# Optimization experiments

Measured on AMD Instinct MI355X. Metric: run time of the kernel, lower is better.

Reference implementation:

```python
import jax, jax.numpy as jnp
import numpy as np

N_NODES = 50000

def gcn_conv(x, src, dst, W, b, n_nodes):
    # PyG GCNConv: add self-loops, symmetric normalization D^-1/2 (A+I) D^-1/2, then bias
    loop = jnp.arange(n_nodes)
    s = jnp.concatenate([src, loop])
    d = jnp.concatenate([dst, loop])
    deg = jax.ops.segment_sum(jnp.ones(s.shape[0], x.dtype), d, num_segments=n_nodes)
    dinv = jnp.where(deg > 0, jax.lax.rsqrt(deg), 0.0)
    norm = dinv[s] * dinv[d]                      # [E+N]
    h = x @ W                                      # [N, out]
    msg = h[s] * norm[:, None]                     # gather + scale
    out = jax.ops.segment_sum(msg, d, num_segments=n_nodes)  # scatter-add
    return out + b

def setup_inputs() -> dict:
    key = jax.random.key(0)
    ks = jax.random.split(key, 8)
    x = jax.random.normal(ks[0], (N_NODES, 128), jnp.float32)
    edge_index = jax.random.randint(ks[1], (2, 800000), 0, N_NODES)
    def glorot(k, fan_in, fan_out):
        lim = np.sqrt(6.0 / (fan_in + fan_out)).astype(np.float32)
        return jax.random.uniform(k, (fan_in, fan_out), jnp.float32, -lim, lim)
    return {
        "x": x,
        "edge_index": edge_index,
        "conv_w1": glorot(ks[2], 128, 64), "conv_b1": jnp.zeros((64,), jnp.float32),
        "conv_w2": glorot(ks[3], 64, 64),  "conv_b2": jnp.zeros((64,), jnp.float32),
        "fc_w1": glorot(ks[4], 64, 32),    "fc_b1": jnp.zeros((32,), jnp.float32),
        "fc_w2": glorot(ks[5], 32, 1),     "fc_b2": jnp.zeros((1,), jnp.float32),
    }

def reference(x, edge_index, conv_w1, conv_b1, conv_w2, conv_b2, fc_w1, fc_b1, fc_w2, fc_b2):
    src, dst = edge_index[0], edge_index[1]
    h = jnp.tanh(gcn_conv(x, src, dst, conv_w1, conv_b1, N_NODES))
    h = jnp.tanh(gcn_conv(h, src, dst, conv_w2, conv_b2, N_NODES))
    h = jnp.tanh(h @ fc_w1 + fc_b1)  # dropout is identity at inference
    return h @ fc_w2 + fc_b2          # [N, 1]
```

## Files before the change

### kernel.cpp

```cpp
#include <hip/hip_runtime.h>
#include <math.h>

#define TPB 256
#define NBK_MAX 512
#define FILL_CAP 4096
#define SC_CH 16

typedef short bf16x8 __attribute__((ext_vector_type(8)));
typedef float f32x4 __attribute__((ext_vector_type(4)));

__device__ __forceinline__ unsigned short rne_bf16(float f) {
  unsigned u = __float_as_uint(f);
  return (unsigned short)((u + 0x7fffu + ((u >> 16) & 1u)) >> 16);
}
__device__ __forceinline__ float bf16_f(unsigned short v) {
  return __uint_as_float((unsigned)v << 16);
}

__global__ __launch_bounds__(TPB) void k_bcount(const int* __restrict__ dst,
                                                int* __restrict__ btot, int E, int NBK) {
  __shared__ int h[NBK_MAX];
  int tid = threadIdx.x, blk = blockIdx.x, G = gridDim.x;
  for (int b = tid; b < NBK; b += TPB) h[b] = 0;
  __syncthreads();
  int chunk = (E + G - 1) / G, lo = blk * chunk, hi = min(E, lo + chunk);
  for (int e = lo + tid; e < hi; e += TPB) atomicAdd(&h[dst[e] >> 7], 1);
  __syncthreads();
  for (int b = tid; b < NBK; b += TPB)
    if (h[b]) atomicAdd(&btot[b], h[b]);
}

__global__ __launch_bounds__(TPB) void k_bstart(const int* __restrict__ btot,
                                                int* __restrict__ bstart,
                                                int* __restrict__ gcur,
                                                int* __restrict__ rowptr,
                                                int NBK, int N, int E) {
  __shared__ int sc[TPB];
  int t = threadIdx.x;
  int i0 = 2 * t, i1 = 2 * t + 1;
  int a0 = (i0 < NBK) ? btot[i0] : 0;
  int a1 = (i1 < NBK) ? btot[i1] : 0;
  int s = a0 + a1;
  sc[t] = s;
  __syncthreads();
  for (int o = 1; o < TPB; o <<= 1) {
    int v = (t >= o) ? sc[t - o] : 0;
    __syncthreads();
    sc[t] += v;
    __syncthreads();
  }
  int excl = sc[t] - s;
  if (i0 < NBK) { bstart[i0] = excl;      gcur[i0] = excl; }
  if (i1 < NBK) { bstart[i1] = excl + a0; gcur[i1] = excl + a0; }
  if (t == 0) { bstart[NBK] = E; rowptr[N] = E; }
}

__global__ __launch_bounds__(TPB) void k_bscatter(const int* __restrict__ src,
                                                  const int* __restrict__ dst,
                                                  int* __restrict__ gcur,
                                                  unsigned* __restrict__ e2,
                                                  int E, int NBK) {
  __shared__ int h[NBK_MAX];
  __shared__ int base[NBK_MAX];
  int tid = threadIdx.x, blk = blockIdx.x, G = gridDim.x;
  int chunk = (E + G - 1) / G, lo = blk * chunk, hi = min(E, lo + chunk);
  for (int t0 = lo; t0 < hi; t0 += TPB * SC_CH) {
    int sv[SC_CH], dv[SC_CH];
    for (int b = tid; b < NBK; b += TPB) h[b] = 0;
    __syncthreads();
#pragma unroll
    for (int u = 0; u < SC_CH; ++u) {
      int e = t0 + u * TPB + tid;
      if (e < hi) {
        dv[u] = dst[e];
        sv[u] = src[e];
        atomicAdd(&h[dv[u] >> 7], 1);
      } else {
        dv[u] = -1;
      }
    }
    __syncthreads();
    for (int b = tid; b < NBK; b += TPB) {
      int c = h[b];
      base[b] = c ? atomicAdd(&gcur[b], c) : 0;
    }
    __syncthreads();
    for (int b = tid; b < NBK; b += TPB) h[b] = 0;
    __syncthreads();
#pragma unroll
    for (int u = 0; u < SC_CH; ++u) {
      if (dv[u] >= 0) {
        int bk = dv[u] >> 7;
        int r = atomicAdd(&h[bk], 1);
        e2[base[bk] + r] = ((unsigned)sv[u] << 7) | (unsigned)(dv[u] & 127);
      }
    }
    __syncthreads();
  }
}

__global__ __launch_bounds__(TPB) void k_build(const unsigned* __restrict__ e2,
                                               const int* __restrict__ bstart,
                                               int* __restrict__ rowptr,
                                               float* __restrict__ dinv,
                                               int* __restrict__ col, int N) {
  __shared__ int c[128], sc[128], cur[128];
  __shared__ int buf[FILL_CAP];
  int tid = threadIdx.x, b = blockIdx.x;
  int st = bstart[b], en = bstart[b + 1], len = en - st;
  if (tid < 128) c[tid] = 0;
  __syncthreads();
  for (int i = st + tid; i < en; i += TPB) atomicAdd(&c[e2[i] & 127u], 1);
  __syncthreads();
  if (tid < 128) sc[tid] = c[tid];
  __syncthreads();
  for (int o = 1; o < 128; o <<= 1) {
    int v = (tid >= o && tid < 128) ? sc[tid - o] : 0;
    __syncthreads();
    if (tid < 128) sc[tid] += v;
    __syncthreads();
  }
  if (tid < 128) {
    int excl = sc[tid] - c[tid];
    cur[tid] = excl;
    int node = b * 128 + tid;
    if (node < N) {
      rowptr[node] = st + excl;
      dinv[node] = rsqrtf((float)(c[tid] + 1));
    }
  }
  __syncthreads();
  if (len <= FILL_CAP) {
    for (int i = st + tid; i < en; i += TPB) {
      unsigned v = e2[i];
      int p = atomicAdd(&cur[v & 127u], 1);
      buf[p] = (int)(v >> 7);
    }
    __syncthreads();
    for (int i = tid; i < len; i += TPB) col[st + i] = buf[i];
  } else {
    for (int i = st + tid; i < en; i += TPB) {
      unsigned v = e2[i];
      int p = atomicAdd(&cur[v & 127u], 1);
      col[st + p] = (int)(v >> 7);
    }
  }
}

__global__ __launch_bounds__(TPB) void k_wsplit2(const float* __restrict__ W1,
                                                 const float* __restrict__ W2,
                                                 unsigned short* __restrict__ hi1,
                                                 unsigned short* __restrict__ lo1,
                                                 unsigned short* __restrict__ hi2,
                                                 unsigned short* __restrict__ lo2) {
  int i = blockIdx.x * TPB + threadIdx.x;
  if (i < 128 * 64) {
    int k = i >> 6, n = i & 63;
    float w = W1[i];
    unsigned short h = rne_bf16(w);
    hi1[n * 128 + k] = h;
    lo1[n * 128 + k] = rne_bf16(w - bf16_f(h));
  } else if (i < 128 * 64 + 64 * 64) {
    int j = i - 128 * 64;
    int k = j >> 6, n = j & 63;
    float w = W2[j];
    unsigned short h = rne_bf16(w);
    hi2[n * 64 + k] = h;
    lo2[n * 64 + k] = rne_bf16(w - bf16_f(h));
  }
}

template <int K, bool AF32>
__global__ __launch_bounds__(TPB) void k_mm(const void* __restrict__ Ap,
                                            const unsigned short* __restrict__ WThi,
                                            const unsigned short* __restrict__ WTlo,
                                            unsigned short* __restrict__ Hout, int N) {
  constexpr int P = K + 8;
  __shared__ unsigned short sHi[64 * P];
  __shared__ unsigned short sLo[64 * P];
  int tid = threadIdx.x;
  constexpr int CH = 64 * K / 8;
  for (int i = tid; i < CH; i += TPB) {
    int n = i / (K / 8), ko = i % (K / 8);
    *(int4*)(sHi + n * P + ko * 8) = *(const int4*)(WThi + n * K + ko * 8);
    *(int4*)(sLo + n * P + ko * 8) = *(const int4*)(WTlo + n * K + ko * 8);
  }
  __syncthreads();
  int wave = tid >> 6, lane = tid & 63;
  int oct = lane >> 4, l15 = lane & 15;
  int base = blockIdx.x * 64 + wave * 16;
  int arow = base + l15;
  if (arow >= N) arow = N - 1;
  f32x4 acc[4] = {};
#pragma unroll
  for (int s = 0; s < K / 32; ++s) {
    bf16x8 ahi, alo;
    if (AF32) {
      const float* ap = (const float*)Ap + (size_t)arow * K + s * 32 + oct * 8;
      float4 f0 = *(const float4*)ap;
      float4 f1 = *(const float4*)(ap + 4);
      float fv[8] = {f0.x, f0.y, f0.z, f0.w, f1.x, f1.y, f1.z, f1.w};
#pragma unroll
      for (int j = 0; j < 8; ++j) {
        unsigned short hb = rne_bf16(fv[j]);
        ahi[j] = (short)hb;
        alo[j] = (short)rne_bf16(fv[j] - bf16_f(hb));
      }
    } else {
      ahi = *(const bf16x8*)((const unsigned short*)Ap + (size_t)arow * K + s * 32 + oct * 8);
    }
#pragma unroll
    for (int t = 0; t < 4; ++t) {
      bf16x8 bhi = *(const bf16x8*)(sHi + (t * 16 + l15) * P + s * 32 + oct * 8);
      bf16x8 blo = *(const bf16x8*)(sLo + (t * 16 + l15) * P + s * 32 + oct * 8);
      acc[t] = __builtin_amdgcn_mfma_f32_16x16x32_bf16(ahi, bhi, acc[t], 0, 0, 0);
      acc[t] = __builtin_amdgcn_mfma_f32_16x16x32_bf16(ahi, blo, acc[t], 0, 0, 0);
      if (AF32)
        acc[t] = __builtin_amdgcn_mfma_f32_16x16x32_bf16(alo, bhi, acc[t], 0, 0, 0);
    }
  }
#pragma unroll
  for (int r = 0; r < 4; ++r) {
    int row = base + oct * 4 + r;
    if (row < N) {
#pragma unroll
      for (int t = 0; t < 4; ++t)
        Hout[(size_t)row * 64 + t * 16 + l15] = rne_bf16(acc[t][r]);
    }
  }
}

__device__ __forceinline__ float rl_f(float v, int l) {
  return __int_as_float(__builtin_amdgcn_readlane(__float_as_int(v), l));
}

__global__ __launch_bounds__(TPB) void k_agg(const unsigned short* __restrict__ H,
                                             const int* __restrict__ rowptr,
                                             const int* __restrict__ col,
                                             const float* __restrict__ dinv,
                                             const float* __restrict__ bias,
                                             unsigned short* __restrict__ OUT, int N) {
  int i = (blockIdx.x * TPB + threadIdx.x) >> 6;
  int lane = threadIdx.x & 63;
  if (i >= N) return;
  float di = dinv[i];
  float acc = bf16_f(H[((size_t)i << 6) + lane]) * di * di;
  int beg = rowptr[i], end = rowptr[i + 1];
  for (int c0 = beg; c0 < end; c0 += 64) {
    int m = end - c0;
    if (m > 64) m = 64;
    int jj = c0 + lane;
    int sv = col[jj < end ? jj : beg];
    float nv = di * dinv[sv];
    int t = 0;
    for (; t + 8 <= m; t += 8) {
      int s0 = __builtin_amdgcn_readlane(sv, t + 0);
      int s1 = __builtin_amdgcn_readlane(sv, t + 1);
      int s2 = __builtin_amdgcn_readlane(sv, t + 2);
      int s3 = __builtin_amdgcn_readlane(sv, t + 3);
      int s4 = __builtin_amdgcn_readlane(sv, t + 4);
      int s5 = __builtin_amdgcn_readlane(sv, t + 5);
      int s6 = __builtin_amdgcn_readlane(sv, t + 6);
      int s7 = __builtin_amdgcn_readlane(sv, t + 7);
      float h0 = bf16_f(H[((size_t)s0 << 6) + lane]);
      float h1 = bf16_f(H[((size_t)s1 << 6) + lane]);
      float h2 = bf16_f(H[((size_t)s2 << 6) + lane]);
      float h3 = bf16_f(H[((size_t)s3 << 6) + lane]);
      float h4 = bf16_f(H[((size_t)s4 << 6) + lane]);
      float h5 = bf16_f(H[((size_t)s5 << 6) + lane]);
      float h6 = bf16_f(H[((size_t)s6 << 6) + lane]);
      float h7 = bf16_f(H[((size_t)s7 << 6) + lane]);
      acc += h0 * rl_f(nv, t + 0);
      acc += h1 * rl_f(nv, t + 1);
      acc += h2 * rl_f(nv, t + 2);
      acc += h3 * rl_f(nv, t + 3);
      acc += h4 * rl_f(nv, t + 4);
      acc += h5 * rl_f(nv, t + 5);
      acc += h6 * rl_f(nv, t + 6);
      acc += h7 * rl_f(nv, t + 7);
    }
    if (t + 4 <= m) {
      int s0 = __builtin_amdgcn_readlane(sv, t + 0);
      int s1 = __builtin_amdgcn_readlane(sv, t + 1);
      int s2 = __builtin_amdgcn_readlane(sv, t + 2);
      int s3 = __builtin_amdgcn_readlane(sv, t + 3);
      float h0 = bf16_f(H[((size_t)s0 << 6) + lane]);
      float h1 = bf16_f(H[((size_t)s1 << 6) + lane]);
      float h2 = bf16_f(H[((size_t)s2 << 6) + lane]);
      float h3 = bf16_f(H[((size_t)s3 << 6) + lane]);
      acc += h0 * rl_f(nv, t + 0);
      acc += h1 * rl_f(nv, t + 1);
      acc += h2 * rl_f(nv, t + 2);
      acc += h3 * rl_f(nv, t + 3);
      t += 4;
    }
    for (; t < m; ++t) {
      int s = __builtin_amdgcn_readlane(sv, t);
      acc += bf16_f(H[((size_t)s << 6) + lane]) * rl_f(nv, t);
    }
  }
  acc += bias[lane];
  OUT[((size_t)i << 6) + lane] = rne_bf16(tanhf(acc));
}

__global__ __launch_bounds__(TPB) void k_fc(const unsigned short* __restrict__ A,
                                            const float* __restrict__ w1,
                                            const float* __restrict__ b1,
                                            const float* __restrict__ w2,
                                            const float* __restrict__ b2,
                                            float* __restrict__ out, int N) {
  __shared__ float sw1t[32 * 64];
  __shared__ float sb1[32];
  __shared__ float sw2[32];
  __shared__ float sA[128 * 65];
  int tid = threadIdx.x;
  for (int i = tid; i < 32 * 64; i += TPB) {
    int j = i >> 6, k = i & 63;
    sw1t[i] = w1[k * 32 + j];
  }
  if (tid < 32) { sb1[tid] = b1[tid]; sw2[tid] = w2[tid]; }
  int base = blockIdx.x * 128;
  for (int i = tid; i < 128 * 64; i += TPB) {
    int r = i >> 6, c = i & 63;
    int g = base + r;
    sA[r * 65 + c] = (g < N) ? bf16_f(A[(size_t)g * 64 + c]) : 0.f;
  }
  __syncthreads();
  int r = tid >> 1, q = tid & 1;
  int node = base + r;
  const float* arow = &sA[r * 65];
  float o = 0.f;
  for (int j = q * 16; j < q * 16 + 16; ++j) {
    float accj = sb1[j];
    const float* wrow = &sw1t[j * 64];
#pragma unroll 8
    for (int k = 0; k < 64; ++k) accj += arow[k] * wrow[k];
    o += tanhf(accj) * sw2[j];
  }
  o += __shfl_xor(o, 1);
  if (q == 0 && node < N) out[node] = o + b2[0];
}

extern "C" void kernel_launch(void* const* d_in, const int* in_sizes, int n_in,
                              void* d_out, int out_size, void* d_ws, size_t ws_size,
                              hipStream_t stream) {
  const float* x   = (const float*)d_in[0];
  const int*   ei  = (const int*)d_in[1];
  const float* w1  = (const float*)d_in[2];
  const float* b1  = (const float*)d_in[3];
  const float* w2  = (const float*)d_in[4];
  const float* b2  = (const float*)d_in[5];
  const float* fw1 = (const float*)d_in[6];
  const float* fb1 = (const float*)d_in[7];
  const float* fw2 = (const float*)d_in[8];
  const float* fb2 = (const float*)d_in[9];
  float* out = (float*)d_out;

  int N = in_sizes[0] / 128;
  int E = in_sizes[1] / 2;
  const int* src = ei;
  const int* dst = ei + E;

  const int G   = 256;
  const int NBK = (N + 127) / 128;

  char* p = (char*)d_ws;
  size_t off = 0;
  auto take = [&](size_t bytes) -> void* {
    void* r = p + off;
    off += (bytes + 255) & ~(size_t)255;
    return r;
  };
  int*            btot   = (int*)take((size_t)NBK * 4);
  int*            bstart = (int*)take((size_t)(NBK + 1) * 4);
  int*            gcur   = (int*)take((size_t)NBK * 4);
  int*            rowptr = (int*)take((size_t)(N + 1) * 4);
  float*          dinv   = (float*)take((size_t)N * 4);
  unsigned*       e2     = (unsigned*)take((size_t)E * 4);
  int*            col    = (int*)take((size_t)E * 4);
  unsigned short* wt1hi  = (unsigned short*)take(64 * 128 * 2);
  unsigned short* wt1lo  = (unsigned short*)take(64 * 128 * 2);
  unsigned short* wt2hi  = (unsigned short*)take(64 * 64 * 2);
  unsigned short* wt2lo  = (unsigned short*)take(64 * 64 * 2);
  unsigned short* h      = (unsigned short*)take((size_t)N * 64 * 2);
  unsigned short* a      = (unsigned short*)take((size_t)N * 64 * 2);
  (void)ws_size; (void)n_in; (void)out_size;

  hipMemsetAsync(btot, 0, (size_t)NBK * 4, stream);
  k_bcount<<<G, TPB, 0, stream>>>(dst, btot, E, NBK);
  k_bstart<<<1, TPB, 0, stream>>>(btot, bstart, gcur, rowptr, NBK, N, E);
  k_bscatter<<<G, TPB, 0, stream>>>(src, dst, gcur, e2, E, NBK);
  k_build<<<NBK, TPB, 0, stream>>>(e2, bstart, rowptr, dinv, col, N);

  k_wsplit2<<<48, TPB, 0, stream>>>(w1, w2, wt1hi, wt1lo, wt2hi, wt2lo);

  int gmm = (N + 63) / 64;
  k_mm<128, true><<<gmm, TPB, 0, stream>>>(x, wt1hi, wt1lo, h, N);
  k_agg<<<(N + 3) / 4, TPB, 0, stream>>>(h, rowptr, col, dinv, b1, a, N);
  k_mm<64, false><<<gmm, TPB, 0, stream>>>(a, wt2hi, wt2lo, h, N);
  k_agg<<<(N + 3) / 4, TPB, 0, stream>>>(h, rowptr, col, dinv, b2, a, N);
  k_fc<<<(N + 127) / 128, TPB, 0, stream>>>(a, fw1, fb1, fw2, fb2, out, N);
}
```

Measured before the change: 218.2 us.

## Fuse all GCN stages into one persistent cooperative kernel with grid syncs

```diff
diff --git a/kernel.cpp b/kernel.cpp
--- a/kernel.cpp
+++ b/kernel.cpp
@@ -1,10 +1,14 @@
 #include <hip/hip_runtime.h>
+#include <hip/hip_cooperative_groups.h>
 #include <math.h>
+
+namespace cg = cooperative_groups;
 
 #define TPB 256
 #define NBK_MAX 512
 #define FILL_CAP 4096
 #define SC_CH 16
+#define SMEM_BYTES 34816
 
 typedef short bf16x8 __attribute__((ext_vector_type(8)));
 typedef float f32x4 __attribute__((ext_vector_type(4)));
@@ -16,26 +20,49 @@
 __device__ __forceinline__ float bf16_f(unsigned short v) {
   return __uint_as_float((unsigned)v << 16);
 }
-
-__global__ __launch_bounds__(TPB) void k_bcount(const int* __restrict__ dst,
-                                                int* __restrict__ btot, int E, int NBK) {
-  __shared__ int h[NBK_MAX];
-  int tid = threadIdx.x, blk = blockIdx.x, G = gridDim.x;
-  for (int b = tid; b < NBK; b += TPB) h[b] = 0;
+__device__ __forceinline__ float rl_f(float v, int l) {
+  return __int_as_float(__builtin_amdgcn_readlane(__float_as_int(v), l));
+}
+
+
+__device__ void bcount_phase(const int* dst, int* btot, int E, int NBK,
+                             int GB, int blk, char* smem) {
+  int* hh = (int*)smem;
+  int tid = threadIdx.x;
+  for (int b = tid; b < NBK; b += TPB) hh[b] = 0;
   __syncthreads();
-  int chunk = (E + G - 1) / G, lo = blk * chunk, hi = min(E, lo + chunk);
-  for (int e = lo + tid; e < hi; e += TPB) atomicAdd(&h[dst[e] >> 7], 1);
+  int chunk = (E + GB - 1) / GB, lo = blk * chunk, hi = min(E, lo + chunk);
+  for (int e = lo + tid; e < hi; e += TPB) atomicAdd(&hh[dst[e] >> 7], 1);
   __syncthreads();
   for (int b = tid; b < NBK; b += TPB)
-    if (h[b]) atomicAdd(&btot[b], h[b]);
-}
-
-__global__ __launch_bounds__(TPB) void k_bstart(const int* __restrict__ btot,
-                                                int* __restrict__ bstart,
-                                                int* __restrict__ gcur,
-                                                int* __restrict__ rowptr,
-                                                int NBK, int N, int E) {
-  __shared__ int sc[TPB];
+    if (hh[b]) atomicAdd(&btot[b], hh[b]);
+}
+
+__device__ void wsplit_phase(const float* W1, const float* W2,
+                             unsigned short* hi1, unsigned short* lo1,
+                             unsigned short* hi2, unsigned short* lo2,
+                             int GB, int blk) {
+  for (int i = blk * TPB + threadIdx.x; i < 128 * 64 + 64 * 64; i += GB * TPB) {
+    if (i < 128 * 64) {
+      int k = i >> 6, n = i & 63;
+      float w = W1[i];
+      unsigned short hb = rne_bf16(w);
+      hi1[n * 128 + k] = hb;
+      lo1[n * 128 + k] = rne_bf16(w - bf16_f(hb));
+    } else {
+      int j = i - 128 * 64;
+      int k = j >> 6, n = j & 63;
+      float w = W2[j];
+      unsigned short hb = rne_bf16(w);
+      hi2[n * 64 + k] = hb;
+      lo2[n * 64 + k] = rne_bf16(w - bf16_f(hb));
+    }
+  }
+}
+
+__device__ void bstart_phase(const int* btot, int* bstart, int* gcur,
+                             int* rowptr, int NBK, int N, int E, char* smem) {
+  int* sc = (int*)smem;
   int t = threadIdx.x;
   int i0 = 2 * t, i1 = 2 * t + 1;
   int a0 = (i0 < NBK) ? btot[i0] : 0;
@@ -53,20 +80,19 @@
   if (i0 < NBK) { bstart[i0] = excl;      gcur[i0] = excl; }
   if (i1 < NBK) { bstart[i1] = excl + a0; gcur[i1] = excl + a0; }
   if (t == 0) { bstart[NBK] = E; rowptr[N] = E; }
-}
-
-__global__ __launch_bounds__(TPB) void k_bscatter(const int* __restrict__ src,
-                                                  const int* __restrict__ dst,
-                                                  int* __restrict__ gcur,
-                                                  unsigned* __restrict__ e2,
-                                                  int E, int NBK) {
-  __shared__ int h[NBK_MAX];
-  __shared__ int base[NBK_MAX];
-  int tid = threadIdx.x, blk = blockIdx.x, G = gridDim.x;
-  int chunk = (E + G - 1) / G, lo = blk * chunk, hi = min(E, lo + chunk);
+  __syncthreads();
+}
+
+__device__ void bscatter_phase(const int* src, const int* dst, int* gcur,
+                               unsigned* e2, int E, int NBK,
+                               int GB, int blk, char* smem) {
+  int* hh = (int*)smem;
+  int* base = hh + NBK_MAX;
+  int tid = threadIdx.x;
+  int chunk = (E + GB - 1) / GB, lo = blk * chunk, hi = min(E, lo + chunk);
   for (int t0 = lo; t0 < hi; t0 += TPB * SC_CH) {
     int sv[SC_CH], dv[SC_CH];
-    for (int b = tid; b < NBK; b += TPB) h[b] = 0;
+    for (int b = tid; b < NBK; b += TPB) hh[b] = 0;
     __syncthreads();
 #pragma unroll
     for (int u = 0; u < SC_CH; ++u) {
@@ -74,24 +100,24 @@
       if (e < hi) {
         dv[u] = dst[e];
         sv[u] = src[e];
-        atomicAdd(&h[dv[u] >> 7], 1);
+        atomicAdd(&hh[dv[u] >> 7], 1);
       } else {
         dv[u] = -1;
       }
     }
     __syncthreads();
     for (int b = tid; b < NBK; b += TPB) {
-      int c = h[b];
+      int c = hh[b];
       base[b] = c ? atomicAdd(&gcur[b], c) : 0;
     }
     __syncthreads();
-    for (int b = tid; b < NBK; b += TPB) h[b] = 0;
+    for (int b = tid; b < NBK; b += TPB) hh[b] = 0;
     __syncthreads();
 #pragma unroll
     for (int u = 0; u < SC_CH; ++u) {
       if (dv[u] >= 0) {
         int bk = dv[u] >> 7;
-        int r = atomicAdd(&h[bk], 1);
+        int r = atomicAdd(&hh[bk], 1);
         e2[base[bk] + r] = ((unsigned)sv[u] << 7) | (unsigned)(dv[u] & 127);
       }
     }
@@ -99,85 +125,63 @@
   }
 }
 
-__global__ __launch_bounds__(TPB) void k_build(const unsigned* __restrict__ e2,
-                                               const int* __restrict__ bstart,
-                                               int* __restrict__ rowptr,
-                                               float* __restrict__ dinv,
-                                               int* __restrict__ col, int N) {
-  __shared__ int c[128], sc[128], cur[128];
-  __shared__ int buf[FILL_CAP];
-  int tid = threadIdx.x, b = blockIdx.x;
-  int st = bstart[b], en = bstart[b + 1], len = en - st;
-  if (tid < 128) c[tid] = 0;
-  __syncthreads();
-  for (int i = st + tid; i < en; i += TPB) atomicAdd(&c[e2[i] & 127u], 1);
-  __syncthreads();
-  if (tid < 128) sc[tid] = c[tid];
-  __syncthreads();
-  for (int o = 1; o < 128; o <<= 1) {
-    int v = (tid >= o && tid < 128) ? sc[tid - o] : 0;
-    __syncthreads();
-    if (tid < 128) sc[tid] += v;
-    __syncthreads();
-  }
-  if (tid < 128) {
-    int excl = sc[tid] - c[tid];
-    cur[tid] = excl;
-    int node = b * 128 + tid;
-    if (node < N) {
-      rowptr[node] = st + excl;
-      dinv[node] = rsqrtf((float)(c[tid] + 1));
-    }
-  }
-  __syncthreads();
-  if (len <= FILL_CAP) {
-    for (int i = st + tid; i < en; i += TPB) {
-      unsigned v = e2[i];
-      int p = atomicAdd(&cur[v & 127u], 1);
-      buf[p] = (int)(v >> 7);
-    }
-    __syncthreads();
-    for (int i = tid; i < len; i += TPB) col[st + i] = buf[i];
-  } else {
-    for (int i = st + tid; i < en; i += TPB) {
-      unsigned v = e2[i];
-      int p = atomicAdd(&cur[v & 127u], 1);
-      col[st + p] = (int)(v >> 7);
-    }
-  }
-}
-
-__global__ __launch_bounds__(TPB) void k_wsplit2(const float* __restrict__ W1,
-                                                 const float* __restrict__ W2,
-                                                 unsigned short* __restrict__ hi1,
-                                                 unsigned short* __restrict__ lo1,
-                                                 unsigned short* __restrict__ hi2,
-                                                 unsigned short* __restrict__ lo2) {
-  int i = blockIdx.x * TPB + threadIdx.x;
-  if (i < 128 * 64) {
-    int k = i >> 6, n = i & 63;
-    float w = W1[i];
-    unsigned short h = rne_bf16(w);
-    hi1[n * 128 + k] = h;
-    lo1[n * 128 + k] = rne_bf16(w - bf16_f(h));
-  } else if (i < 128 * 64 + 64 * 64) {
-    int j = i - 128 * 64;
-    int k = j >> 6, n = j & 63;
-    float w = W2[j];
-    unsigned short h = rne_bf16(w);
-    hi2[n * 64 + k] = h;
-    lo2[n * 64 + k] = rne_bf16(w - bf16_f(h));
+__device__ void build_phase(const unsigned* e2, const int* bstart, int* rowptr,
+                            float* dinv, int* col, int N, int NBK, char* smem) {
+  int* c = (int*)smem;
+  int* sc = c + 128;
+  int* cur = c + 256;
+  int* buf = c + 384;
+  int tid = threadIdx.x;
+  for (int b = blockIdx.x; b < NBK; b += gridDim.x) {
+    __syncthreads();
+    if (tid < 128) c[tid] = 0;
+    __syncthreads();
+    int st = bstart[b], en = bstart[b + 1], len = en - st;
+    for (int i = st + tid; i < en; i += TPB) atomicAdd(&c[e2[i] & 127u], 1);
+    __syncthreads();
+    if (tid < 128) sc[tid] = c[tid];
+    __syncthreads();
+    for (int o = 1; o < 128; o <<= 1) {
+      int v = (tid >= o && tid < 128) ? sc[tid - o] : 0;
+      __syncthreads();
+      if (tid < 128) sc[tid] += v;
+      __syncthreads();
+    }
+    if (tid < 128) {
+      int excl = sc[tid] - c[tid];
+      cur[tid] = excl;
+      int node = b * 128 + tid;
+      if (node < N) {
+        rowptr[node] = st + excl;
+        dinv[node] = rsqrtf((float)(c[tid] + 1));
+      }
+    }
+    __syncthreads();
+    if (len <= FILL_CAP) {
+      for (int i = st + tid; i < en; i += TPB) {
+        unsigned v = e2[i];
+        int p2 = atomicAdd(&cur[v & 127u], 1);
+        buf[p2] = (int)(v >> 7);
+      }
+      __syncthreads();
+      for (int i = tid; i < len; i += TPB) col[st + i] = buf[i];
+    } else {
+      for (int i = st + tid; i < en; i += TPB) {
+        unsigned v = e2[i];
+        int p2 = atomicAdd(&cur[v & 127u], 1);
+        col[st + p2] = (int)(v >> 7);
+      }
+    }
   }
 }
 
 template <int K, bool AF32>
-__global__ __launch_bounds__(TPB) void k_mm(const void* __restrict__ Ap,
-                                            const unsigned short* __restrict__ WThi,
-                                            const unsigned short* __restrict__ WTlo,
-                                            unsigned short* __restrict__ Hout, int N) {
+__device__ void mm_phase(const void* Ap, const unsigned short* WThi,
+                         const unsigned short* WTlo, unsigned short* Hout,
+                         int N, char* smem) {
   constexpr int P = K + 8;
-  __shared__ unsigned short sHi[64 * P];
-  __shared__ unsigned short sLo[64 * P];
+  unsigned short* sHi = (unsigned short*)smem;
+  unsigned short* sLo = sHi + 64 * P;
   int tid = threadIdx.x;
   constexpr int CH = 64 * K / 8;
   for (int i = tid; i < CH; i += TPB) {
@@ -188,216 +192,343 @@
   __syncthreads();
   int wave = tid >> 6, lane = tid & 63;
   int oct = lane >> 4, l15 = lane & 15;
-  int base = blockIdx.x * 64 + wave * 16;
-  int arow = base + l15;
-  if (arow >= N) arow = N - 1;
-  f32x4 acc[4] = {};
-#pragma unroll
-  for (int s = 0; s < K / 32; ++s) {
-    bf16x8 ahi, alo;
-    if (AF32) {
-      const float* ap = (const float*)Ap + (size_t)arow * K + s * 32 + oct * 8;
-      float4 f0 = *(const float4*)ap;
-      float4 f1 = *(const float4*)(ap + 4);
-      float fv[8] = {f0.x, f0.y, f0.z, f0.w, f1.x, f1.y, f1.z, f1.w};
-#pragma unroll
-      for (int j = 0; j < 8; ++j) {
-        unsigned short hb = rne_bf16(fv[j]);
-        ahi[j] = (short)hb;
-        alo[j] = (short)rne_bf16(fv[j] - bf16_f(hb));
-      }
-    } else {
-      ahi = *(const bf16x8*)((const unsigned short*)Ap + (size_t)arow * K + s * 32 + oct * 8);
-    }
-#pragma unroll
-    for (int t = 0; t < 4; ++t) {
-      bf16x8 bhi = *(const bf16x8*)(sHi + (t * 16 + l15) * P + s * 32 + oct * 8);
-      bf16x8 blo = *(const bf16x8*)(sLo + (t * 16 + l15) * P + s * 32 + oct * 8);
-      acc[t] = __builtin_amdgcn_mfma_f32_16x16x32_bf16(ahi, bhi, acc[t], 0, 0, 0);
-      acc[t] = __builtin_amdgcn_mfma_f32_16x16x32_bf16(ahi, blo, acc[t], 0, 0, 0);
-      if (AF32)
-        acc[t] = __builtin_amdgcn_mfma_f32_16x16x32_bf16(alo, bhi, acc[t], 0, 0, 0);
-    }
-  }
-#pragma unroll
-  for (int r = 0; r < 4; ++r) {
-    int row = base + oct * 4 + r;
-    if (row < N) {
-#pragma unroll
-      for (int t = 0; t < 4; ++t)
-        Hout[(size_t)row * 64 + t * 16 + l15] = rne_bf16(acc[t][r]);
-    }
-  }
-}
-
-__device__ __forceinline__ float rl_f(float v, int l) {
-  return __int_as_float(__builtin_amdgcn_readlane(__float_as_int(v), l));
-}
-
-__global__ __launch_bounds__(TPB) void k_agg(const unsigned short* __restrict__ H,
-                                             const int* __restrict__ rowptr,
-                                             const int* __restrict__ col,
-                                             const float* __restrict__ dinv,
-                                             const float* __restrict__ bias,
-                                             unsigned short* __restrict__ OUT, int N) {
-  int i = (blockIdx.x * TPB + threadIdx.x) >> 6;
+  for (int tb = blockIdx.x * 64; tb < N; tb += gridDim.x * 64) {
+    int base = tb + wave * 16;
+    int arow = base + l15;
+    if (arow >= N) arow = N - 1;
+    f32x4 acc[4] = {};
+#pragma unroll
+    for (int s = 0; s < K / 32; ++s) {
+      bf16x8 ahi, alo;
+      if (AF32) {
+        const float* ap = (const float*)Ap + (size_t)arow * K + s * 32 + oct * 8;
+        float4 f0 = *(const float4*)ap;
+        float4 f1 = *(const float4*)(ap + 4);
+        float fv[8] = {f0.x, f0.y, f0.z, f0.w, f1.x, f1.y, f1.z, f1.w};
+#pragma unroll
+        for (int j = 0; j < 8; ++j) {
+          unsigned short hb = rne_bf16(fv[j]);
+          ahi[j] = (short)hb;
+          alo[j] = (short)rne_bf16(fv[j] - bf16_f(hb));
+        }
+      } else {
+        ahi = *(const bf16x8*)((const unsigned short*)Ap + (size_t)arow * K + s * 32 + oct * 8);
+      }
+#pragma unroll
+      for (int t = 0; t < 4; ++t) {
+        bf16x8 bhi = *(const bf16x8*)(sHi + (t * 16 + l15) * P + s * 32 + oct * 8);
+        bf16x8 blo = *(const bf16x8*)(sLo + (t * 16 + l15) * P + s * 32 + oct * 8);
+        acc[t] = __builtin_amdgcn_mfma_f32_16x16x32_bf16(ahi, bhi, acc[t], 0, 0, 0);
+        acc[t] = __builtin_amdgcn_mfma_f32_16x16x32_bf16(ahi, blo, acc[t], 0, 0, 0);
+        if (AF32)
+          acc[t] = __builtin_amdgcn_mfma_f32_16x16x32_bf16(alo, bhi, acc[t], 0, 0, 0);
+      }
+    }
+#pragma unroll
+    for (int r = 0; r < 4; ++r) {
+      int row = base + oct * 4 + r;
+      if (row < N) {
+#pragma unroll
+        for (int t = 0; t < 4; ++t)
+          Hout[(size_t)row * 64 + t * 16 + l15] = rne_bf16(acc[t][r]);
+      }
+    }
+  }
+}
+
+__device__ void agg_phase(const unsigned short* H, const int* rowptr,
+                          const int* col, const float* dinv, const float* bias,
+                          unsigned short* OUT, int N) {
+  int wid = (blockIdx.x * TPB + threadIdx.x) >> 6;
+  int gw = (gridDim.x * TPB) >> 6;
   int lane = threadIdx.x & 63;
-  if (i >= N) return;
-  float di = dinv[i];
-  float acc = bf16_f(H[((size_t)i << 6) + lane]) * di * di;
-  int beg = rowptr[i], end = rowptr[i + 1];
-  for (int c0 = beg; c0 < end; c0 += 64) {
-    int m = end - c0;
-    if (m > 64) m = 64;
-    int jj = c0 + lane;
-    int sv = col[jj < end ? jj : beg];
-    float nv = di * dinv[sv];
-    int t = 0;
-    for (; t + 8 <= m; t += 8) {
-      int s0 = __builtin_amdgcn_readlane(sv, t + 0);
-      int s1 = __builtin_amdgcn_readlane(sv, t + 1);
-      int s2 = __builtin_amdgcn_readlane(sv, t + 2);
-      int s3 = __builtin_amdgcn_readlane(sv, t + 3);
-      int s4 = __builtin_amdgcn_readlane(sv, t + 4);
-      int s5 = __builtin_amdgcn_readlane(sv, t + 5);
-      int s6 = __builtin_amdgcn_readlane(sv, t + 6);
-      int s7 = __builtin_amdgcn_readlane(sv, t + 7);
-      float h0 = bf16_f(H[((size_t)s0 << 6) + lane]);
-      float h1 = bf16_f(H[((size_t)s1 << 6) + lane]);
-      float h2 = bf16_f(H[((size_t)s2 << 6) + lane]);
-      float h3 = bf16_f(H[((size_t)s3 << 6) + lane]);
-      float h4 = bf16_f(H[((size_t)s4 << 6) + lane]);
-      float h5 = bf16_f(H[((size_t)s5 << 6) + lane]);
-      float h6 = bf16_f(H[((size_t)s6 << 6) + lane]);
-      float h7 = bf16_f(H[((size_t)s7 << 6) + lane]);
-      acc += h0 * rl_f(nv, t + 0);
-      acc += h1 * rl_f(nv, t + 1);
-      acc += h2 * rl_f(nv, t + 2);
-      acc += h3 * rl_f(nv, t + 3);
-      acc += h4 * rl_f(nv, t + 4);
-      acc += h5 * rl_f(nv, t + 5);
-      acc += h6 * rl_f(nv, t + 6);
-      acc += h7 * rl_f(nv, t + 7);
-    }
-    if (t + 4 <= m) {
-      int s0 = __builtin_amdgcn_readlane(sv, t + 0);
-      int s1 = __builtin_amdgcn_readlane(sv, t + 1);
-      int s2 = __builtin_amdgcn_readlane(sv, t + 2);
-      int s3 = __builtin_amdgcn_readlane(sv, t + 3);
-      float h0 = bf16_f(H[((size_t)s0 << 6) + lane]);
-      float h1 = bf16_f(H[((size_t)s1 << 6) + lane]);
-      float h2 = bf16_f(H[((size_t)s2 << 6) + lane]);
-      float h3 = bf16_f(H[((size_t)s3 << 6) + lane]);
-      acc += h0 * rl_f(nv, t + 0);
-      acc += h1 * rl_f(nv, t + 1);
-      acc += h2 * rl_f(nv, t + 2);
-      acc += h3 * rl_f(nv, t + 3);
-      t += 4;
-    }
-    for (; t < m; ++t) {
-      int s = __builtin_amdgcn_readlane(sv, t);
-      acc += bf16_f(H[((size_t)s << 6) + lane]) * rl_f(nv, t);
-    }
-  }
-  acc += bias[lane];
-  OUT[((size_t)i << 6) + lane] = rne_bf16(tanhf(acc));
-}
-
-__global__ __launch_bounds__(TPB) void k_fc(const unsigned short* __restrict__ A,
-                                            const float* __restrict__ w1,
-                                            const float* __restrict__ b1,
-                                            const float* __restrict__ w2,
-                                            const float* __restrict__ b2,
-                                            float* __restrict__ out, int N) {
-  __shared__ float sw1t[32 * 64];
-  __shared__ float sb1[32];
-  __shared__ float sw2[32];
-  __shared__ float sA[128 * 65];
+  float bs = bias[lane];
+  for (int i = wid; i < N; i += gw) {
+    float di = dinv[i];
+    float acc = bf16_f(H[((size_t)i << 6) + lane]) * di * di;
+    int beg = rowptr[i], end = rowptr[i + 1];
+    for (int c0 = beg; c0 < end; c0 += 64) {
+      int m = end - c0;
+      if (m > 64) m = 64;
+      int jj = c0 + lane;
+      int sv = col[jj < end ? jj : beg];
+      float nv = di * dinv[sv];
+      int t = 0;
+      for (; t + 8 <= m; t += 8) {
+        int s0 = __builtin_amdgcn_readlane(sv, t + 0);
+        int s1 = __builtin_amdgcn_readlane(sv, t + 1);
+        int s2 = __builtin_amdgcn_readlane(sv, t + 2);
+        int s3 = __builtin_amdgcn_readlane(sv, t + 3);
+        int s4 = __builtin_amdgcn_readlane(sv, t + 4);
+        int s5 = __builtin_amdgcn_readlane(sv, t + 5);
+        int s6 = __builtin_amdgcn_readlane(sv, t + 6);
+        int s7 = __builtin_amdgcn_readlane(sv, t + 7);
+        float h0 = bf16_f(H[((size_t)s0 << 6) + lane]);
+        float h1 = bf16_f(H[((size_t)s1 << 6) + lane]);
+        float h2 = bf16_f(H[((size_t)s2 << 6) + lane]);
+        float h3 = bf16_f(H[((size_t)s3 << 6) + lane]);
+        float h4 = bf16_f(H[((size_t)s4 << 6) + lane]);
+        float h5 = bf16_f(H[((size_t)s5 << 6) + lane]);
+        float h6 = bf16_f(H[((size_t)s6 << 6) + lane]);
+        float h7 = bf16_f(H[((size_t)s7 << 6) + lane]);
+        acc += h0 * rl_f(nv, t + 0);
+        acc += h1 * rl_f(nv, t + 1);
+        acc += h2 * rl_f(nv, t + 2);
+        acc += h3 * rl_f(nv, t + 3);
+        acc += h4 * rl_f(nv, t + 4);
+        acc += h5 * rl_f(nv, t + 5);
+        acc += h6 * rl_f(nv, t + 6);
+        acc += h7 * rl_f(nv, t + 7);
+      }
+      if (t + 4 <= m) {
+        int s0 = __builtin_amdgcn_readlane(sv, t + 0);
+        int s1 = __builtin_amdgcn_readlane(sv, t + 1);
+        int s2 = __builtin_amdgcn_readlane(sv, t + 2);
+        int s3 = __builtin_amdgcn_readlane(sv, t + 3);
+        float h0 = bf16_f(H[((size_t)s0 << 6) + lane]);
+        float h1 = bf16_f(H[((size_t)s1 << 6) + lane]);
+        float h2 = bf16_f(H[((size_t)s2 << 6) + lane]);
+        float h3 = bf16_f(H[((size_t)s3 << 6) + lane]);
+        acc += h0 * rl_f(nv, t + 0);
+        acc += h1 * rl_f(nv, t + 1);
+        acc += h2 * rl_f(nv, t + 2);
+        acc += h3 * rl_f(nv, t + 3);
+        t += 4;
+      }
+      for (; t < m; ++t) {
+        int s = __builtin_amdgcn_readlane(sv, t);
+        acc += bf16_f(H[((size_t)s << 6) + lane]) * rl_f(nv, t);
+      }
+    }
+    OUT[((size_t)i << 6) + lane] = rne_bf16(tanhf(acc + bs));
+  }
+}
+
+__device__ void fc_phase(const unsigned short* A, const float* w1,
+                         const float* b1, const float* w2, const float* b2,
+                         float* out, int N, char* smem) {
+  float* sw1t = (float*)smem;
+  float* sb1 = sw1t + 32 * 64;
+  float* sw2 = sb1 + 32;
   int tid = threadIdx.x;
   for (int i = tid; i < 32 * 64; i += TPB) {
     int j = i >> 6, k = i & 63;
     sw1t[i] = w1[k * 32 + j];
   }
   if (tid < 32) { sb1[tid] = b1[tid]; sw2[tid] = w2[tid]; }
-  int base = blockIdx.x * 128;
-  for (int i = tid; i < 128 * 64; i += TPB) {
-    int r = i >> 6, c = i & 63;
-    int g = base + r;
-    sA[r * 65 + c] = (g < N) ? bf16_f(A[(size_t)g * 64 + c]) : 0.f;
-  }
   __syncthreads();
-  int r = tid >> 1, q = tid & 1;
-  int node = base + r;
-  const float* arow = &sA[r * 65];
-  float o = 0.f;
-  for (int j = q * 16; j < q * 16 + 16; ++j) {
-    float accj = sb1[j];
-    const float* wrow = &sw1t[j * 64];
-#pragma unroll 8
-    for (int k = 0; k < 64; ++k) accj += arow[k] * wrow[k];
-    o += tanhf(accj) * sw2[j];
-  }
-  o += __shfl_xor(o, 1);
-  if (q == 0 && node < N) out[node] = o + b2[0];
-}
+  float bb = b2[0];
+  for (int node = blockIdx.x * TPB + tid; node < N; node += gridDim.x * TPB) {
+    uint4 rv[8];
+    const uint4* ap = (const uint4*)(A + (size_t)node * 64);
+#pragma unroll
+    for (int q = 0; q < 8; ++q) rv[q] = ap[q];
+    float o = 0.f;
+    for (int j = 0; j < 32; ++j) {
+      const float* wr = sw1t + j * 64;
+      float accj = sb1[j];
+#pragma unroll
+      for (int q = 0; q < 8; ++q) {
+        unsigned u0 = rv[q].x, u1 = rv[q].y, u2 = rv[q].z, u3 = rv[q].w;
+        accj += __uint_as_float(u0 << 16) * wr[8 * q + 0] +
+                __uint_as_float(u0 & 0xffff0000u) * wr[8 * q + 1];
+        accj += __uint_as_float(u1 << 16) * wr[8 * q + 2] +
+                __uint_as_float(u1 & 0xffff0000u) * wr[8 * q + 3];
+        accj += __uint_as_float(u2 << 16) * wr[8 * q + 4] +
+                __uint_as_float(u2 & 0xffff0000u) * wr[8 * q + 5];
+        accj += __uint_as_float(u3 << 16) * wr[8 * q + 6] +
+                __uint_as_float(u3 & 0xffff0000u) * wr[8 * q + 7];
+      }
+      o += tanhf(accj) * sw2[j];
+    }
+    out[node] = o + bb;
+  }
+}
+
+
+struct KParams {
+  const float* x;
+  const int* src;
+  const int* dst;
+  const float* w1;
+  const float* b1;
+  const float* w2;
+  const float* b2;
+  const float* fw1;
+  const float* fb1;
+  const float* fw2;
+  const float* fb2;
+  float* out;
+  int* btot;
+  int* bstart;
+  int* gcur;
+  int* rowptr;
+  float* dinv;
+  unsigned* e2;
+  int* col;
+  unsigned short* wt1hi;
+  unsigned short* wt1lo;
+  unsigned short* wt2hi;
+  unsigned short* wt2lo;
+  unsigned short* hbuf;
+  unsigned short* abuf;
+  int N, E, NBK;
+};
+
+__global__ __launch_bounds__(TPB, 4) void k_all(KParams p) {
+  __shared__ __align__(16) char smem[SMEM_BYTES];
+  cg::grid_group grid = cg::this_grid();
+  const int blk = blockIdx.x;
+  const int G = gridDim.x;
+  const int GB = (G < 256) ? G : 256;
+
+  if (blk == 0)
+    for (int b = threadIdx.x; b < p.NBK; b += TPB) p.btot[b] = 0;
+  grid.sync();
+
+  if (blk < GB) {
+    bcount_phase(p.dst, p.btot, p.E, p.NBK, GB, blk, smem);
+    wsplit_phase(p.w1, p.w2, p.wt1hi, p.wt1lo, p.wt2hi, p.wt2lo, GB, blk);
+  }
+  grid.sync();
+
+  if (blk == 0)
+    bstart_phase(p.btot, p.bstart, p.gcur, p.rowptr, p.NBK, p.N, p.E, smem);
+  mm_phase<128, true>(p.x, p.wt1hi, p.wt1lo, p.hbuf, p.N, smem);
+  grid.sync();
+
+  if (blk < GB)
+    bscatter_phase(p.src, p.dst, p.gcur, p.e2, p.E, p.NBK, GB, blk, smem);
+  grid.sync();
+
+  build_phase(p.e2, p.bstart, p.rowptr, p.dinv, p.col, p.N, p.NBK, smem);
+  grid.sync();
+
+  agg_phase(p.hbuf, p.rowptr, p.col, p.dinv, p.b1, p.abuf, p.N);
+  grid.sync();
+
+  mm_phase<64, false>(p.abuf, p.wt2hi, p.wt2lo, p.hbuf, p.N, smem);
+  grid.sync();
+
+  agg_phase(p.hbuf, p.rowptr, p.col, p.dinv, p.b2, p.abuf, p.N);
+  grid.sync();
+
+  fc_phase(p.abuf, p.fw1, p.fb1, p.fw2, p.fb2, p.out, p.N, smem);
+}
+
+
+__global__ __launch_bounds__(TPB) void kf_bcount(const int* dst, int* btot, int E, int NBK) {
+  __shared__ __align__(16) char smem[NBK_MAX * 4];
+  bcount_phase(dst, btot, E, NBK, gridDim.x, blockIdx.x, smem);
+}
+__global__ __launch_bounds__(TPB) void kf_wsplit(const float* w1, const float* w2,
+                                                 unsigned short* a, unsigned short* b,
+                                                 unsigned short* c, unsigned short* d) {
+  wsplit_phase(w1, w2, a, b, c, d, gridDim.x, blockIdx.x);
+}
+__global__ __launch_bounds__(TPB) void kf_bstart(const int* btot, int* bstart, int* gcur,
+                                                 int* rowptr, int NBK, int N, int E) {
+  __shared__ __align__(16) char smem[TPB * 4];
+  bstart_phase(btot, bstart, gcur, rowptr, NBK, N, E, smem);
+}
+__global__ __launch_bounds__(TPB) void kf_bscatter(const int* src, const int* dst, int* gcur,
+                                                   unsigned* e2, int E, int NBK) {
+  __shared__ __align__(16) char smem[NBK_MAX * 8];
+  bscatter_phase(src, dst, gcur, e2, E, NBK, gridDim.x, blockIdx.x, smem);
+}
+__global__ __launch_bounds__(TPB) void kf_build(const unsigned* e2, const int* bstart,
+                                                int* rowptr, float* dinv, int* col,
+                                                int N, int NBK) {
+  __shared__ __align__(16) char smem[(384 + FILL_CAP) * 4];
+  build_phase(e2, bstart, rowptr, dinv, col, N, NBK, smem);
+}
+__global__ __launch_bounds__(TPB) void kf_mm128(const float* X, const unsigned short* hi,
+                                                const unsigned short* lo, unsigned short* H, int N) {
+  __shared__ __align__(16) char smem[SMEM_BYTES];
+  mm_phase<128, true>(X, hi, lo, H, N, smem);
+}
+__global__ __launch_bounds__(TPB) void kf_mm64(const unsigned short* X, const unsigned short* hi,
+                                               const unsigned short* lo, unsigned short* H, int N) {
+  __shared__ __align__(16) char smem[64 * 72 * 2 * 2];
+  mm_phase<64, false>(X, hi, lo, H, N, smem);
+}
+__global__ __launch_bounds__(TPB) void kf_agg(const unsigned short* H, const int* rowptr,
+                                              const int* col, const float* dinv,
+                                              const float* bias, unsigned short* OUT, int N) {
+  agg_phase(H, rowptr, col, dinv, bias, OUT, N);
+}
+__global__ __launch_bounds__(TPB) void kf_fc(const unsigned short* A, const float* w1,
+                                             const float* b1, const float* w2,
+                                             const float* b2, float* out, int N) {
+  __shared__ __align__(16) char smem[(32 * 64 + 64) * 4];
+  fc_phase(A, w1, b1, w2, b2, out, N, smem);
+}
+
 
 extern "C" void kernel_launch(void* const* d_in, const int* in_sizes, int n_in,
                               void* d_out, int out_size, void* d_ws, size_t ws_size,
                               hipStream_t stream) {
-  const float* x   = (const float*)d_in[0];
-  const int*   ei  = (const int*)d_in[1];
-  const float* w1  = (const float*)d_in[2];
-  const float* b1  = (const float*)d_in[3];
-  const float* w2  = (const float*)d_in[4];
-  const float* b2  = (const float*)d_in[5];
-  const float* fw1 = (const float*)d_in[6];
-  const float* fb1 = (const float*)d_in[7];
-  const float* fw2 = (const float*)d_in[8];
-  const float* fb2 = (const float*)d_in[9];
-  float* out = (float*)d_out;
-
-  int N = in_sizes[0] / 128;
-  int E = in_sizes[1] / 2;
-  const int* src = ei;
-  const int* dst = ei + E;
-
-  const int G   = 256;
-  const int NBK = (N + 127) / 128;
-
-  char* p = (char*)d_ws;
+  KParams p;
+  p.x   = (const float*)d_in[0];
+  const int* ei = (const int*)d_in[1];
+  p.w1  = (const float*)d_in[2];
+  p.b1  = (const float*)d_in[3];
+  p.w2  = (const float*)d_in[4];
+  p.b2  = (const float*)d_in[5];
+  p.fw1 = (const float*)d_in[6];
+  p.fb1 = (const float*)d_in[7];
+  p.fw2 = (const float*)d_in[8];
+  p.fb2 = (const float*)d_in[9];
+  p.out = (float*)d_out;
+
+  p.N = in_sizes[0] / 128;
+  p.E = in_sizes[1] / 2;
+  p.src = ei;
+  p.dst = ei + p.E;
+  p.NBK = (p.N + 127) / 128;
+
+  char* wp = (char*)d_ws;
   size_t off = 0;
   auto take = [&](size_t bytes) -> void* {
-    void* r = p + off;
+    void* r = wp + off;
     off += (bytes + 255) & ~(size_t)255;
     return r;
   };
-  int*            btot   = (int*)take((size_t)NBK * 4);
-  int*            bstart = (int*)take((size_t)(NBK + 1) * 4);
-  int*            gcur   = (int*)take((size_t)NBK * 4);
-  int*            rowptr = (int*)take((size_t)(N + 1) * 4);
-  float*          dinv   = (float*)take((size_t)N * 4);
-  unsigned*       e2     = (unsigned*)take((size_t)E * 4);
-  int*            col    = (int*)take((size_t)E * 4);
-  unsigned short* wt1hi  = (unsigned short*)take(64 * 128 * 2);
-  unsigned short* wt1lo  = (unsigned short*)take(64 * 128 * 2);
-  unsigned short* wt2hi  = (unsigned short*)take(64 * 64 * 2);
-  unsigned short* wt2lo  = (unsigned short*)take(64 * 64 * 2);
-  unsigned short* h      = (unsigned short*)take((size_t)N * 64 * 2);
-  unsigned short* a      = (unsigned short*)take((size_t)N * 64 * 2);
+  p.btot   = (int*)take((size_t)p.NBK * 4);
+  p.bstart = (int*)take((size_t)(p.NBK + 1) * 4);
+  p.gcur   = (int*)take((size_t)p.NBK * 4);
+  p.rowptr = (int*)take((size_t)(p.N + 1) * 4);
+  p.dinv   = (float*)take((size_t)p.N * 4);
+  p.e2     = (unsigned*)take((size_t)p.E * 4);
+  p.col    = (int*)take((size_t)p.E * 4);
+  p.wt1hi  = (unsigned short*)take(64 * 128 * 2);
+  p.wt1lo  = (unsigned short*)take(64 * 128 * 2);
+  p.wt2hi  = (unsigned short*)take(64 * 64 * 2);
+  p.wt2lo  = (unsigned short*)take(64 * 64 * 2);
+  p.hbuf   = (unsigned short*)take((size_t)p.N * 64 * 2);
+  p.abuf   = (unsigned short*)take((size_t)p.N * 64 * 2);
   (void)ws_size; (void)n_in; (void)out_size;
 
-  hipMemsetAsync(btot, 0, (size_t)NBK * 4, stream);
-  k_bcount<<<G, TPB, 0, stream>>>(dst, btot, E, NBK);
-  k_bstart<<<1, TPB, 0, stream>>>(btot, bstart, gcur, rowptr, NBK, N, E);
-  k_bscatter<<<G, TPB, 0, stream>>>(src, dst, gcur, e2, E, NBK);
-  k_build<<<NBK, TPB, 0, stream>>>(e2, bstart, rowptr, dinv, col, N);
-
-  k_wsplit2<<<48, TPB, 0, stream>>>(w1, w2, wt1hi, wt1lo, wt2hi, wt2lo);
-
-  int gmm = (N + 63) / 64;
-  k_mm<128, true><<<gmm, TPB, 0, stream>>>(x, wt1hi, wt1lo, h, N);
-  k_agg<<<(N + 3) / 4, TPB, 0, stream>>>(h, rowptr, col, dinv, b1, a, N);
-  k_mm<64, false><<<gmm, TPB, 0, stream>>>(a, wt2hi, wt2lo, h, N);
-  k_agg<<<(N + 3) / 4, TPB, 0, stream>>>(h, rowptr, col, dinv, b2, a, N);
-  k_fc<<<(N + 127) / 128, TPB, 0, stream>>>(a, fw1, fb1, fw2, fb2, out, N);
-}
+  int maxb = 0;
+  hipError_t oe = hipOccupancyMaxActiveBlocksPerMultiprocessor(&maxb, k_all, TPB, 0);
+  if (oe != hipSuccess || maxb < 1) maxb = 1;
+  int nblk = maxb * 256;
+  if (nblk > 1024) nblk = 1024;
+  void* args[] = {(void*)&p};
+  hipError_t err = hipLaunchCooperativeKernel((const void*)k_all, dim3(nblk), dim3(TPB),
+                                              args, 0, stream);
+  if (err == hipSuccess) return;
+
+  hipMemsetAsync(p.btot, 0, (size_t)p.NBK * 4, stream);
+  kf_bcount<<<256, TPB, 0, stream>>>(p.dst, p.btot, p.E, p.NBK);
+  kf_wsplit<<<64, TPB, 0, stream>>>(p.w1, p.w2, p.wt1hi, p.wt1lo, p.wt2hi, p.wt2lo);
+  kf_bstart<<<1, TPB, 0, stream>>>(p.btot, p.bstart, p.gcur, p.rowptr, p.NBK, p.N, p.E);
+  kf_bscatter<<<256, TPB, 0, stream>>>(p.src, p.dst, p.gcur, p.e2, p.E, p.NBK);
+  kf_build<<<p.NBK, TPB, 0, stream>>>(p.e2, p.bstart, p.rowptr, p.dinv, p.col, p.N, p.NBK);
+  int gmm = (p.N + 63) / 64;
+  kf_mm128<<<gmm, TPB, 0, stream>>>(p.x, p.wt1hi, p.wt1lo, p.hbuf, p.N);
+  kf_agg<<<(p.N + 3) / 4, TPB, 0, stream>>>(p.hbuf, p.rowptr, p.col, p.dinv, p.b1, p.abuf, p.N);
+  kf_mm64<<<gmm, TPB, 0, stream>>>(p.abuf, p.wt2hi, p.wt2lo, p.hbuf, p.N);
+  kf_agg<<<(p.N + 3) / 4, TPB, 0, stream>>>(p.hbuf, p.rowptr, p.col, p.dinv, p.b2, p.abuf, p.N);
+  kf_fc<<<(p.N + 255) / 256, TPB, 0, stream>>>(p.abuf, p.fw1, p.fb1, p.fw2, p.fb2, p.out, p.N);
+}
```

New measurement: 734.8 us. 3.37x slower.
